# Kernel tuning notes

Measured on AMD Instinct MI355X. Metric: run time of the kernel, lower is better.

## Reference

```python
import math
import jax, jax.numpy as jnp
import numpy as np

EMBED_DIM = 2048
NUM_HEADS = 16
NUM_KV_HEADS = 8
DEPTH = 12
HEAD_DIM = EMBED_DIM // NUM_HEADS // 2  # 64
N_REP = NUM_HEADS // NUM_KV_HEADS       # 2
SCALING = HEAD_DIM ** (-0.5)
LAMBDA_INIT = 0.8 - 0.6 * math.exp(-0.3 * DEPTH)
EPS = 1e-5


def _rope_cos_sin(seq_len, head_dim, offset=0):
    pos = jnp.arange(offset, offset + seq_len, dtype=jnp.float32)
    theta = jnp.arange(0, head_dim, 2, dtype=jnp.float32) / head_dim
    inv_freq = 1.0 / (10000.0 ** theta + 1e-8)
    sinusoid = pos[:, None] * inv_freq[None, :]  # [seq, head_dim//2]
    return jnp.cos(sinusoid), jnp.sin(sinusoid)


def _apply_rotary_interleaved(x, cos, sin):
    # x: [b, s, h, d]; cos/sin: [s, d//2]; interleaved pairs (even, odd)
    x1 = x[..., 0::2]
    x2 = x[..., 1::2]
    c = cos[None, :, None, :]
    s = sin[None, :, None, :]
    o1 = x1 * c - x2 * s
    o2 = x1 * s + x2 * c
    return jnp.stack([o1, o2], axis=-1).reshape(x.shape)


def setup_inputs() -> dict:
    key = jax.random.key(0)
    ks = jax.random.split(key, 12)
    d = EMBED_DIM
    inp = {
        "q": jax.random.normal(ks[0], (1, 2048, d), dtype=jnp.float32),
        "k": jax.random.normal(ks[1], (1, 2048, d), dtype=jnp.float32),
        "v": jax.random.normal(ks[2], (1, 2048, d), dtype=jnp.float32),
        "Wq": jax.random.normal(ks[3], (d, d), dtype=jnp.float32) * (d ** -0.5),
        "Wk": jax.random.normal(ks[4], (d, d // N_REP), dtype=jnp.float32) * (d ** -0.5),
        "Wv": jax.random.normal(ks[5], (d, d // N_REP), dtype=jnp.float32) * (d ** -0.5),
        "Wout": jax.random.normal(ks[6], (d, d), dtype=jnp.float32) * (d ** -0.5),
        "lq1": jax.random.normal(ks[7], (HEAD_DIM,), dtype=jnp.float32) * 0.1,
        "lk1": jax.random.normal(ks[8], (HEAD_DIM,), dtype=jnp.float32) * 0.1,
        "lq2": jax.random.normal(ks[9], (HEAD_DIM,), dtype=jnp.float32) * 0.1,
        "lk2": jax.random.normal(ks[10], (HEAD_DIM,), dtype=jnp.float32) * 0.1,
        "subln_w": jnp.ones((2 * HEAD_DIM,), dtype=jnp.float32),
    }
    return inp


def reference(q, k, v, Wq, Wk, Wv, Wout, lq1, lk1, lq2, lk2, subln_w):
    bsz, tgt_len, _ = q.shape
    src_len = k.shape[1]
    hd = HEAD_DIM

    qp = (q @ Wq).reshape(bsz, tgt_len, 2 * NUM_HEADS, hd)
    kp = (k @ Wk).reshape(bsz, src_len, 2 * NUM_KV_HEADS, hd)
    vp = (v @ Wv).reshape(bsz, src_len, NUM_KV_HEADS, 2 * hd)

    q_cos, q_sin = _rope_cos_sin(tgt_len, hd)
    k_cos, k_sin = _rope_cos_sin(src_len, hd)
    qp = _apply_rotary_interleaved(qp, q_cos, q_sin)
    kp = _apply_rotary_interleaved(kp, k_cos, k_sin)

    qp = jnp.transpose(qp, (0, 2, 1, 3)) * SCALING          # [b, 2H, t, hd]
    kp = jnp.repeat(jnp.transpose(kp, (0, 2, 1, 3)), N_REP, axis=1)  # [b, 2H, s, hd]
    vp = jnp.repeat(jnp.transpose(vp, (0, 2, 1, 3)), N_REP, axis=1)  # [b, H, s, 2hd]

    attn_weights = jnp.einsum('bhtd,bhsd->bhts', qp, kp)
    attn_weights = jax.nn.softmax(attn_weights.astype(jnp.float32), axis=-1).astype(qp.dtype)

    lambda_1 = jnp.exp(jnp.sum(lq1 * lk1))
    lambda_2 = jnp.exp(jnp.sum(lq2 * lk2))
    lambda_full = lambda_1 - lambda_2 + LAMBDA_INIT

    attn_weights = attn_weights.reshape(bsz, NUM_HEADS, 2, tgt_len, src_len)
    attn_weights = attn_weights[:, :, 0] - lambda_full * attn_weights[:, :, 1]

    attn = jnp.einsum('bhts,bhsd->bhtd', attn_weights, vp)  # [b, H, t, 2hd]

    # RMSNorm over last dim with affine weight
    rms = jax.lax.rsqrt(jnp.mean(jnp.square(attn), axis=-1, keepdims=True) + EPS)
    attn = attn * rms * subln_w
    attn = attn * (1.0 - LAMBDA_INIT)

    attn = jnp.transpose(attn, (0, 2, 1, 3)).reshape(bsz, tgt_len, NUM_HEADS * 2 * hd)
    return attn @ Wout
```

## Files before the change

### kernel.cpp

```cpp
#include <hip/hip_runtime.h>

typedef unsigned short u16;
typedef unsigned int u32;
typedef float f32x4 __attribute__((ext_vector_type(4)));
typedef float f32x2 __attribute__((ext_vector_type(2)));
typedef unsigned int u32x2 __attribute__((ext_vector_type(2)));
typedef __bf16 bf16x8 __attribute__((ext_vector_type(8)));
typedef __bf16 bf16x4 __attribute__((ext_vector_type(4)));

#define LAMBDA_INIT_F 0.7836057665316245f
#define ONE_MINUS_LI  0.2163942334683755f
#define THR_LOG2 11.0f
#define Q_SCALE 0.18033688011112042f

__device__ __forceinline__ u16 f2b(float f) {
  union { float f; u32 u; } x; x.f = f;
  u32 r = x.u + 0x7fffu + ((x.u >> 16) & 1u);
  return (u16)(r >> 16);
}

__device__ __forceinline__ f32x4 mfma16(bf16x8 a, bf16x8 b, f32x4 c) {
  return __builtin_amdgcn_mfma_f32_16x16x32_bf16(a, b, c, 0, 0, 0);
}

__device__ __forceinline__ float fexp2(float x) { return __builtin_amdgcn_exp2f(x); }

__device__ __forceinline__ void gll16(const void* gp, void* lp) {
  __builtin_amdgcn_global_load_lds((__attribute__((address_space(1))) void*)(gp),
                                   (__attribute__((address_space(3))) void*)(lp),
                                   16, 0, 0);
}

__global__ __launch_bounds__(256) void cast3_kernel(const float* __restrict__ q,
                                                    const float* __restrict__ k,
                                                    const float* __restrict__ v,
                                                    u16* __restrict__ qb,
                                                    u16* __restrict__ kb,
                                                    u16* __restrict__ vb,
                                                    f32x2* __restrict__ tbl) {
  int bid = blockIdx.x;
  if (bid >= 6144) {
    int idx = (bid - 6144) * 256 + threadIdx.x;
    int t = idx >> 5, j = idx & 31;
    float theta = (float)j * (1.0f / 32.0f);
    float denom = expf(theta * 9.210340371976184f);
    float invf = 1.0f / (denom + 1e-8f);
    float ang = (float)t * invf;
    tbl[idx] = (f32x2){cosf(ang), sinf(ang)};
    return;
  }
  int seg = bid >> 11;
  int i = (bid & 2047) * 256 + threadIdx.x;
  const float* in = seg == 0 ? q : (seg == 1 ? k : v);
  u16* out = seg == 0 ? qb : (seg == 1 ? kb : vb);
  const f32x4* p = (const f32x4*)(in + (size_t)i * 8);
  f32x4 a = p[0], b = p[1];
  union { u16 u[8]; f32x4 v; } o;
#pragma unroll
  for (int j = 0; j < 4; ++j) { o.u[j] = f2b(a[j]); o.u[4 + j] = f2b(b[j]); }
  *(f32x4*)(out + (size_t)i * 8) = o.v;
}

__device__ __forceinline__ void trans_body(const float* __restrict__ in,
                                           u16* __restrict__ out, int R, int C) {
  __shared__ float tile[32][33];
  int bx = blockIdx.x * 32;
  int by = blockIdx.y * 32;
  int tx = threadIdx.x & 31, ty = threadIdx.x >> 5;
#pragma unroll
  for (int i = 0; i < 32; i += 8)
    tile[ty + i][tx] = in[(size_t)(by + ty + i) * C + bx + tx];
  __syncthreads();
#pragma unroll
  for (int i = 0; i < 32; i += 8)
    out[(size_t)(bx + ty + i) * R + by + tx] = f2b(tile[tx][ty + i]);
}

__global__ __launch_bounds__(256) void wtrans_kernel(
    const float* __restrict__ Wq, u16* __restrict__ WqT,
    const float* __restrict__ Wk, u16* __restrict__ WkT,
    const float* __restrict__ Wv, u16* __restrict__ WvT,
    const float* __restrict__ Wo, u16* __restrict__ WoT) {
  int z = blockIdx.z;
  const float* in;
  u16* out;
  int C;
  if (z == 0)      { in = Wq; out = WqT; C = 2048; }
  else if (z == 1) { in = Wk; out = WkT; C = 1024; }
  else if (z == 2) { in = Wv; out = WvT; C = 1024; }
  else             { in = Wo; out = WoT; C = 2048; }
  if (blockIdx.x * 32 >= C) return;
  trans_body(in, out, 2048, C);
}

template <int MODE>
__device__ __forceinline__ void gemm_body(u16* As, u16* Bs,
                                          const u16* __restrict__ A,
                                          const u16* __restrict__ Bt,
                                          void* __restrict__ Cout,
                                          const f32x2* __restrict__ tbl,
                                          float scale,
                                          int N, int K, int bx, int by) {
  const int tid = threadIdx.x;
  const int lane = tid & 63;
  const int wave = tid >> 6;
  const int m0 = by * 128;
  const int n0 = bx * 128;
  const int wm = (wave >> 1) * 64;
  const int wn = (wave & 1) * 64;
  const int g = lane >> 4, c = lane & 15;

  f32x4 acc[4][4];
#pragma unroll
  for (int i = 0; i < 4; ++i)
#pragma unroll
    for (int j = 0; j < 4; ++j) acc[i][j] = (f32x4){0.f, 0.f, 0.f, 0.f};

  for (int k0 = 0; k0 < K; k0 += 64) {
    __syncthreads();
#pragma unroll
    for (int it = 0; it < 4; ++it) {
      int gi = it * 256 + tid;
      int R = gi >> 3;
      int lg = (gi & 7) ^ (R & 7);
      gll16(A + (size_t)(m0 + R) * K + k0 + lg * 8, As + gi * 8);
      gll16(Bt + (size_t)(n0 + R) * K + k0 + lg * 8, Bs + gi * 8);
    }
    __syncthreads();
#pragma unroll
    for (int kk = 0; kk < 2; ++kk) {
      bf16x8 af[4], bf[4];
#pragma unroll
      for (int i = 0; i < 4; ++i) {
        int ph = ((kk * 4 + g) ^ (c & 7)) * 8;
        af[i] = *(const bf16x8*)&As[(wm + i * 16 + c) * 64 + ph];
        bf[i] = *(const bf16x8*)&Bs[(wn + i * 16 + c) * 64 + ph];
      }
#pragma unroll
      for (int i = 0; i < 4; ++i)
#pragma unroll
        for (int j = 0; j < 4; ++j) acc[i][j] = mfma16(af[i], bf[j], acc[i][j]);
    }
  }

  if constexpr (MODE == 0) {
    float* C = (float*)Cout;
#pragma unroll
    for (int i = 0; i < 4; ++i)
#pragma unroll
      for (int j = 0; j < 4; ++j) {
        int mrow = m0 + wm + i * 16 + g * 4;
        int ncol = n0 + wn + j * 16 + c;
#pragma unroll
        for (int r = 0; r < 4; ++r) C[(size_t)(mrow + r) * N + ncol] = acc[i][j][r];
      }
  } else if constexpr (MODE == 1) {
    u16* Oh = (u16*)Cout;
    const bool even = (c & 1) == 0;
#pragma unroll
    for (int i = 0; i < 4; ++i)
#pragma unroll
      for (int j = 0; j < 4; ++j) {
        int mrow = m0 + wm + i * 16 + g * 4;
        int ncol = n0 + wn + j * 16 + c;
        int hh = ncol >> 6;
        int d = ncol & 63;
        int jd = d >> 1;
        f32x4 own = acc[i][j];
        f32x4 part;
#pragma unroll
        for (int r = 0; r < 4; ++r) part[r] = __shfl_xor(own[r], 1);
        if (even) {
#pragma unroll
          for (int r = 0; r < 4; ++r) {
            f32x2 cs = tbl[(mrow + r) * 32 + jd];
            float o1 = (own[r] * cs[0] - part[r] * cs[1]) * scale;
            float o2 = (own[r] * cs[1] + part[r] * cs[0]) * scale;
            u32 pk = (u32)f2b(o1) | ((u32)f2b(o2) << 16);
            *(u32*)&Oh[((size_t)hh * 2048 + mrow + r) * 64 + d] = pk;
          }
        }
      }
  } else {
    u16* Vt = (u16*)Cout;
#pragma unroll
    for (int i = 0; i < 4; ++i)
#pragma unroll
      for (int j = 0; j < 4; ++j) {
        int ncol = n0 + wn + j * 16 + c;
        int tblk = (m0 + wm + i * 16) >> 5;
        int p0 = 8 * g + 4 * (i & 1);
        u32x2 pk;
        pk[0] = (u32)f2b(acc[i][j][0]) | ((u32)f2b(acc[i][j][1]) << 16);
        pk[1] = (u32)f2b(acc[i][j][2]) | ((u32)f2b(acc[i][j][3]) << 16);
        *(u32x2*)&Vt[(size_t)ncol * 2048 + tblk * 32 + p0] = pk;
      }
  }
}

__global__ __launch_bounds__(256, 2) void gemm_qkv_kernel(
    const u16* __restrict__ qb, const u16* __restrict__ WqT, u16* __restrict__ Qh,
    const u16* __restrict__ kb, const u16* __restrict__ WkT, u16* __restrict__ Kh,
    const u16* __restrict__ vb, const u16* __restrict__ WvT, u16* __restrict__ Vt,
    const f32x2* __restrict__ tbl) {
  __shared__ u16 As[128 * 64];
  __shared__ u16 Bs[128 * 64];
  int bid = ((blockIdx.x & 7) << 6) | (blockIdx.x >> 3);
  if (bid < 256) {
    gemm_body<1>(As, Bs, qb, WqT, Qh, tbl, Q_SCALE, 2048, 2048, bid & 15, bid >> 4);
  } else if (bid < 384) {
    int t = bid - 256;
    gemm_body<1>(As, Bs, kb, WkT, Kh, tbl, 1.0f, 1024, 2048, t & 7, t >> 3);
  } else {
    int t = bid - 384;
    gemm_body<2>(As, Bs, vb, WvT, Vt, tbl, 1.0f, 1024, 2048, t & 7, t >> 3);
  }
}

__global__ __launch_bounds__(256, 2) void gemm_one_kernel(const u16* __restrict__ A,
                                                          const u16* __restrict__ Bt,
                                                          float* __restrict__ C) {
  __shared__ u16 As[128 * 64];
  __shared__ u16 Bs[128 * 64];
  int bid = ((blockIdx.x & 7) << 5) | (blockIdx.x >> 3);
  gemm_body<0>(As, Bs, A, Bt, C, nullptr, 1.0f, 2048, 2048, bid & 15, bid >> 4);
}

__global__ __launch_bounds__(512, 2) void attn_kernel(const u16* __restrict__ Qb,
                                                      const u16* __restrict__ Kb,
                                                      const u16* __restrict__ Vt,
                                                      u16* __restrict__ AO,
                                                      const float* __restrict__ lq1,
                                                      const float* __restrict__ lk1,
                                                      const float* __restrict__ lq2,
                                                      const float* __restrict__ lk2,
                                                      const float* __restrict__ subln) {
  const int b = ((blockIdx.x & 7) << 5) | (blockIdx.x >> 3);
  const int h = b >> 4;
  const int tid = threadIdx.x;
  const int wave = tid >> 6;
  const int lane = tid & 63;
  const int t0 = ((b & 15) * 8 + wave) * 16;
  const int g = lane >> 4, c = lane & 15;
  const int c7 = c & 7;

  __shared__ u16 smem[24576];

  const u16* Kh = Kb + (size_t)h * 2048 * 64;
  const u16* Vh = Vt + (size_t)(h >> 1) * 128 * 2048;

  float myl1 = lq1[lane] * lk1[lane];
  float myl2 = lq2[lane] * lk2[lane];
#pragma unroll
  for (int off = 32; off; off >>= 1) {
    myl1 += __shfl_xor(myl1, off);
    myl2 += __shfl_xor(myl2, off);
  }
  const float lambda_full = expf(myl1) - expf(myl2) + LAMBDA_INIT_F;

  bf16x8 qf[2][2];
#pragma unroll
  for (int e = 0; e < 2; ++e)
#pragma unroll
    for (int d = 0; d < 2; ++d)
      qf[e][d] = *(const bf16x8*)(Qb + ((size_t)(2 * h + e) * 2048 + t0 + c) * 64 + d * 32 + g * 8);

  const int kb0 = c * 64 + ((g ^ c7) * 8);
  const int kb1 = kb0 ^ 32;

  const u16* ksrc0;
  const u16* vsrc0;
  const u16* vsrc1;
  { int gi = tid;       int R = gi >> 3; ksrc0 = Kh + R * 64 + ((gi & 7) ^ (R & 7)) * 8; }
  { int gi = tid;       int R = gi >> 3; vsrc0 = Vh + (size_t)R * 2048 + ((gi & 7) ^ (R & 7)) * 8; }
  { int gi = 512 + tid; int R = gi >> 3; vsrc1 = Vh + (size_t)R * 2048 + ((gi & 7) ^ (R & 7)) * 8; }

  f32x4 O[2][8];
#pragma unroll
  for (int e = 0; e < 2; ++e)
#pragma unroll
    for (int f = 0; f < 8; ++f) O[e][f] = (f32x4){0.f, 0.f, 0.f, 0.f};
  float m0 = -1e30f, m1 = -1e30f, ls0 = 0.f, ls1 = 0.f;

#define STAGE(kOff, vOff, s0)                                   \
  do {                                                          \
    gll16(ksrc0 + (size_t)(s0) * 64, smem + (kOff) + tid * 8);  \
    gll16(vsrc0 + (s0), smem + (vOff) + tid * 8);               \
    gll16(vsrc1 + (s0), smem + (vOff) + 4096 + tid * 8);        \
  } while (0)

#define TILE(kOff, vOff)                                                      \
  do {                                                                        \
    bf16x8 kf[4][2];                                                          \
    _Pragma("unroll") for (int sf = 0; sf < 4; ++sf) {                        \
      kf[sf][0] = *(const bf16x8*)&smem[(kOff) + kb0 + sf * 1024];            \
      kf[sf][1] = *(const bf16x8*)&smem[(kOff) + kb1 + sf * 1024];            \
    }                                                                         \
    f32x4 sa[2][4];                                                           \
    _Pragma("unroll") for (int e = 0; e < 2; ++e)                             \
      _Pragma("unroll") for (int sf = 0; sf < 4; ++sf) {                      \
        f32x4 z = (f32x4){0.f, 0.f, 0.f, 0.f};                                \
        z = mfma16(kf[sf][0], qf[e][0], z);                                   \
        z = mfma16(kf[sf][1], qf[e][1], z);                                   \
        sa[e][sf] = z;                                                        \
      }                                                                       \
    bf16x8 vv0[8];                                                            \
    _Pragma("unroll") for (int f = 0; f < 8; ++f)                             \
      vv0[f] = *(const bf16x8*)&smem[(vOff) + kb0 + f * 1024];                \
    bf16x8 paf[2][2];                                                         \
    _Pragma("unroll") for (int e = 0; e < 2; ++e) {                           \
      float& m_e = e ? m1 : m0;                                               \
      float& ls_e = e ? ls1 : ls0;                                            \
      float mx = sa[e][0][0];                                                 \
      _Pragma("unroll") for (int sf = 0; sf < 4; ++sf)                        \
        _Pragma("unroll") for (int r = 0; r < 4; ++r)                         \
          mx = fmaxf(mx, sa[e][sf][r]);                                       \
      mx = fmaxf(mx, __shfl_xor(mx, 16));                                     \
      mx = fmaxf(mx, __shfl_xor(mx, 32));                                     \
      if (__any(mx > m_e + THR_LOG2)) {                                       \
        float mn = fmaxf(m_e, mx);                                            \
        float sc = fexp2(m_e - mn);                                           \
        m_e = mn;                                                             \
        ls_e *= sc;                                                           \
        float scr[4];                                                         \
        _Pragma("unroll") for (int r = 0; r < 4; ++r) scr[r] = __shfl(sc, g * 4 + r); \
        _Pragma("unroll") for (int ff = 0; ff < 8; ++ff)                      \
          _Pragma("unroll") for (int r = 0; r < 4; ++r) O[e][ff][r] *= scr[r]; \
      }                                                                       \
      float p[4][4];                                                          \
      float sum = 0.f;                                                        \
      _Pragma("unroll") for (int sf = 0; sf < 4; ++sf)                        \
        _Pragma("unroll") for (int r = 0; r < 4; ++r) {                       \
          float pv = fexp2(sa[e][sf][r] - m_e);                               \
          p[sf][r] = pv;                                                      \
          sum += pv;                                                          \
        }                                                                     \
      sum += __shfl_xor(sum, 16);                                             \
      sum += __shfl_xor(sum, 32);                                             \
      ls_e += sum;                                                            \
      paf[e][0] = (bf16x8){(__bf16)p[0][0], (__bf16)p[0][1], (__bf16)p[0][2], (__bf16)p[0][3], \
                           (__bf16)p[1][0], (__bf16)p[1][1], (__bf16)p[1][2], (__bf16)p[1][3]}; \
      paf[e][1] = (bf16x8){(__bf16)p[2][0], (__bf16)p[2][1], (__bf16)p[2][2], (__bf16)p[2][3], \
                           (__bf16)p[3][0], (__bf16)p[3][1], (__bf16)p[3][2], (__bf16)p[3][3]}; \
    }                                                                         \
    __builtin_amdgcn_s_setprio(1);                                            \
    bf16x8 vv1[8];                                                            \
    _Pragma("unroll") for (int f = 0; f < 8; ++f)                             \
      vv1[f] = *(const bf16x8*)&smem[(vOff) + kb1 + f * 1024];                \
    _Pragma("unroll") for (int f = 0; f < 8; ++f) {                           \
      O[0][f] = mfma16(paf[0][0], vv0[f], O[0][f]);                           \
      O[1][f] = mfma16(paf[1][0], vv0[f], O[1][f]);                           \
    }                                                                         \
    _Pragma("unroll") for (int f = 0; f < 8; ++f) {                           \
      O[0][f] = mfma16(paf[0][1], vv1[f], O[0][f]);                           \
      O[1][f] = mfma16(paf[1][1], vv1[f], O[1][f]);                           \
    }                                                                         \
    __builtin_amdgcn_s_setprio(0);                                            \
  } while (0)

  STAGE(0, 8192, 0);

#pragma unroll 1
  for (int t = 0; t < 32; t += 2) {
    __syncthreads();
    STAGE(4096, 16384, (t + 1) * 64);
    TILE(0, 8192);
    __syncthreads();
    if (t < 30) STAGE(0, 8192, (t + 2) * 64);
    TILE(4096, 16384);
  }

  float inv0 = 1.f / ls0, inv1 = 1.f / ls1;
  float i0[4], i1[4];
#pragma unroll
  for (int r = 0; r < 4; ++r) {
    i0[r] = __shfl(inv0, g * 4 + r);
    i1[r] = __shfl(inv1, g * 4 + r);
  }
  float res[8][4];
  float ss[4] = {0.f, 0.f, 0.f, 0.f};
#pragma unroll
  for (int f = 0; f < 8; ++f)
#pragma unroll
    for (int r = 0; r < 4; ++r) {
      float vv = O[0][f][r] * i0[r] - lambda_full * (O[1][f][r] * i1[r]);
      res[f][r] = vv;
      ss[r] += vv * vv;
    }
#pragma unroll
  for (int off = 1; off < 16; off <<= 1)
#pragma unroll
    for (int r = 0; r < 4; ++r) ss[r] += __shfl_xor(ss[r], off);
  float rms[4];
#pragma unroll
  for (int r = 0; r < 4; ++r)
    rms[r] = rsqrtf(ss[r] * (1.0f / 128.0f) + 1e-5f) * ONE_MINUS_LI;
  float w[8];
#pragma unroll
  for (int f = 0; f < 8; ++f) w[f] = subln[f * 16 + c];
#pragma unroll
  for (int f = 0; f < 8; ++f)
#pragma unroll
    for (int r = 0; r < 4; ++r)
      AO[(size_t)(t0 + g * 4 + r) * 2048 + h * 128 + f * 16 + c] = f2b(res[f][r] * rms[r] * w[f]);
}

extern "C" void kernel_launch(void* const* d_in, const int* in_sizes, int n_in,
                              void* d_out, int out_size, void* d_ws, size_t ws_size,
                              hipStream_t stream) {
  const float* q     = (const float*)d_in[0];
  const float* k     = (const float*)d_in[1];
  const float* v     = (const float*)d_in[2];
  const float* Wq    = (const float*)d_in[3];
  const float* Wk    = (const float*)d_in[4];
  const float* Wv    = (const float*)d_in[5];
  const float* Wout  = (const float*)d_in[6];
  const float* lq1   = (const float*)d_in[7];
  const float* lk1   = (const float*)d_in[8];
  const float* lq2   = (const float*)d_in[9];
  const float* lk2   = (const float*)d_in[10];
  const float* subln = (const float*)d_in[11];
  float* out = (float*)d_out;

  char* ws = (char*)d_ws;
  size_t off = 0;
  auto alloc = [&](size_t bytes) -> void* {
    void* p = ws + off;
    off += (bytes + 255) & ~(size_t)255;
    return p;
  };
  u16* qb  = (u16*)alloc(2048ull * 2048 * 2);
  u16* kb  = (u16*)alloc(2048ull * 2048 * 2);
  u16* vb  = (u16*)alloc(2048ull * 2048 * 2);
  u16* WqT = (u16*)alloc(2048ull * 2048 * 2);
  u16* WkT = (u16*)alloc(1024ull * 2048 * 2);
  u16* WvT = (u16*)alloc(1024ull * 2048 * 2);
  u16* WoT = (u16*)alloc(2048ull * 2048 * 2);
  f32x2* tbl = (f32x2*)alloc(2048ull * 32 * 8);
  u16* Qh  = (u16*)alloc(32ull * 2048 * 64 * 2);
  u16* Kh  = (u16*)alloc(16ull * 2048 * 64 * 2);
  u16* Vt  = (u16*)alloc(1024ull * 2048 * 2);
  u16* AO  = (u16*)alloc(2048ull * 2048 * 2);

  cast3_kernel<<<6400, 256, 0, stream>>>(q, k, v, qb, kb, vb, tbl);
  wtrans_kernel<<<dim3(64, 64, 4), 256, 0, stream>>>(Wq, WqT, Wk, WkT, Wv, WvT, Wout, WoT);
  gemm_qkv_kernel<<<512, 256, 0, stream>>>(qb, WqT, Qh, kb, WkT, Kh, vb, WvT, Vt, tbl);
  attn_kernel<<<256, 512, 0, stream>>>(Qh, Kh, Vt, AO, lq1, lk1, lq2, lk2, subln);
  gemm_one_kernel<<<256, 256, 0, stream>>>(AO, WoT, out);
}
```

Before: 156.2 us.

## Merge prep kernels and split attention into smaller 4-wave blocks

The input cast, RoPE table and weight-transpose kernels are merged into a single prep launch, removing one kernel launch and the idle wasted blocks of the old 3D transpose grid. The attention kernel now runs 512 blocks of 256 threads, each covering 64 query rows instead of 128, with staging loads spread over four waves. This gives finer scheduling granularity across CUs, but each block now loads K/V tiles for half as many queries, doubling total K/V traffic.

```diff
diff --git a/kernel.cpp b/kernel.cpp
--- a/kernel.cpp
+++ b/kernel.cpp
@@ -31,15 +31,45 @@
                                    16, 0, 0);
 }
 
-__global__ __launch_bounds__(256) void cast3_kernel(const float* __restrict__ q,
-                                                    const float* __restrict__ k,
-                                                    const float* __restrict__ v,
-                                                    u16* __restrict__ qb,
-                                                    u16* __restrict__ kb,
-                                                    u16* __restrict__ vb,
-                                                    f32x2* __restrict__ tbl) {
+__device__ __forceinline__ void trans_body2(const float* __restrict__ in,
+                                            u16* __restrict__ out, int R, int C,
+                                            int bxb, int byb) {
+  __shared__ float tile[32][33];
+  int bx = bxb * 32;
+  int by = byb * 32;
+  int tx = threadIdx.x & 31, ty = threadIdx.x >> 5;
+#pragma unroll
+  for (int i = 0; i < 32; i += 8)
+    tile[ty + i][tx] = in[(size_t)(by + ty + i) * C + bx + tx];
+  __syncthreads();
+#pragma unroll
+  for (int i = 0; i < 32; i += 8)
+    out[(size_t)(bx + ty + i) * R + by + tx] = f2b(tile[tx][ty + i]);
+}
+
+__global__ __launch_bounds__(256) void prep_kernel(
+    const float* __restrict__ q, const float* __restrict__ k, const float* __restrict__ v,
+    u16* __restrict__ qb, u16* __restrict__ kb, u16* __restrict__ vb,
+    f32x2* __restrict__ tbl,
+    const float* __restrict__ Wq, u16* __restrict__ WqT,
+    const float* __restrict__ Wk, u16* __restrict__ WkT,
+    const float* __restrict__ Wv, u16* __restrict__ WvT,
+    const float* __restrict__ Wo, u16* __restrict__ WoT) {
   int bid = blockIdx.x;
-  if (bid >= 6144) {
+  if (bid < 6144) {
+    int seg = bid >> 11;
+    int i = (bid & 2047) * 256 + threadIdx.x;
+    const float* in = seg == 0 ? q : (seg == 1 ? k : v);
+    u16* out = seg == 0 ? qb : (seg == 1 ? kb : vb);
+    const f32x4* p = (const f32x4*)(in + (size_t)i * 8);
+    f32x4 a = p[0], b = p[1];
+    union { u16 u[8]; f32x4 v; } o;
+#pragma unroll
+    for (int j = 0; j < 4; ++j) { o.u[j] = f2b(a[j]); o.u[4 + j] = f2b(b[j]); }
+    *(f32x4*)(out + (size_t)i * 8) = o.v;
+    return;
+  }
+  if (bid < 6400) {
     int idx = (bid - 6144) * 256 + threadIdx.x;
     int t = idx >> 5, j = idx & 31;
     float theta = (float)j * (1.0f / 32.0f);
@@ -49,48 +79,11 @@
     tbl[idx] = (f32x2){cosf(ang), sinf(ang)};
     return;
   }
-  int seg = bid >> 11;
-  int i = (bid & 2047) * 256 + threadIdx.x;
-  const float* in = seg == 0 ? q : (seg == 1 ? k : v);
-  u16* out = seg == 0 ? qb : (seg == 1 ? kb : vb);
-  const f32x4* p = (const f32x4*)(in + (size_t)i * 8);
-  f32x4 a = p[0], b = p[1];
-  union { u16 u[8]; f32x4 v; } o;
-#pragma unroll
-  for (int j = 0; j < 4; ++j) { o.u[j] = f2b(a[j]); o.u[4 + j] = f2b(b[j]); }
-  *(f32x4*)(out + (size_t)i * 8) = o.v;
-}
-
-__device__ __forceinline__ void trans_body(const float* __restrict__ in,
-                                           u16* __restrict__ out, int R, int C) {
-  __shared__ float tile[32][33];
-  int bx = blockIdx.x * 32;
-  int by = blockIdx.y * 32;
-  int tx = threadIdx.x & 31, ty = threadIdx.x >> 5;
-#pragma unroll
-  for (int i = 0; i < 32; i += 8)
-    tile[ty + i][tx] = in[(size_t)(by + ty + i) * C + bx + tx];
-  __syncthreads();
-#pragma unroll
-  for (int i = 0; i < 32; i += 8)
-    out[(size_t)(bx + ty + i) * R + by + tx] = f2b(tile[tx][ty + i]);
-}
-
-__global__ __launch_bounds__(256) void wtrans_kernel(
-    const float* __restrict__ Wq, u16* __restrict__ WqT,
-    const float* __restrict__ Wk, u16* __restrict__ WkT,
-    const float* __restrict__ Wv, u16* __restrict__ WvT,
-    const float* __restrict__ Wo, u16* __restrict__ WoT) {
-  int z = blockIdx.z;
-  const float* in;
-  u16* out;
-  int C;
-  if (z == 0)      { in = Wq; out = WqT; C = 2048; }
-  else if (z == 1) { in = Wk; out = WkT; C = 1024; }
-  else if (z == 2) { in = Wv; out = WvT; C = 1024; }
-  else             { in = Wo; out = WoT; C = 2048; }
-  if (blockIdx.x * 32 >= C) return;
-  trans_body(in, out, 2048, C);
+  int w = bid - 6400;
+  if (w < 4096)      trans_body2(Wq, WqT, 2048, 2048, w & 63, w >> 6);
+  else if (w < 6144) { w -= 4096; trans_body2(Wk, WkT, 2048, 1024, w & 31, w >> 5); }
+  else if (w < 8192) { w -= 6144; trans_body2(Wv, WvT, 2048, 1024, w & 31, w >> 5); }
+  else               { w -= 8192; trans_body2(Wo, WoT, 2048, 2048, w & 63, w >> 6); }
 }
 
 template <int MODE>
@@ -226,7 +219,7 @@
   gemm_body<0>(As, Bs, A, Bt, C, nullptr, 1.0f, 2048, 2048, bid & 15, bid >> 4);
 }
 
-__global__ __launch_bounds__(512, 2) void attn_kernel(const u16* __restrict__ Qb,
+__global__ __launch_bounds__(256, 2) void attn_kernel(const u16* __restrict__ Qb,
                                                       const u16* __restrict__ Kb,
                                                       const u16* __restrict__ Vt,
                                                       u16* __restrict__ AO,
@@ -235,12 +228,12 @@
                                                       const float* __restrict__ lq2,
                                                       const float* __restrict__ lk2,
                                                       const float* __restrict__ subln) {
-  const int b = ((blockIdx.x & 7) << 5) | (blockIdx.x >> 3);
-  const int h = b >> 4;
+  const int b = ((blockIdx.x & 7) << 6) | (blockIdx.x >> 3);
+  const int h = b >> 5;
   const int tid = threadIdx.x;
   const int wave = tid >> 6;
   const int lane = tid & 63;
-  const int t0 = ((b & 15) * 8 + wave) * 16;
+  const int t0 = ((b & 31) * 4 + wave) * 16;
   const int g = lane >> 4, c = lane & 15;
   const int c7 = c & 7;
 
@@ -269,11 +262,17 @@
   const int kb1 = kb0 ^ 32;
 
   const u16* ksrc0;
+  const u16* ksrc1;
   const u16* vsrc0;
   const u16* vsrc1;
+  const u16* vsrc2;
+  const u16* vsrc3;
   { int gi = tid;       int R = gi >> 3; ksrc0 = Kh + R * 64 + ((gi & 7) ^ (R & 7)) * 8; }
+  { int gi = 256 + tid; int R = gi >> 3; ksrc1 = Kh + R * 64 + ((gi & 7) ^ (R & 7)) * 8; }
   { int gi = tid;       int R = gi >> 3; vsrc0 = Vh + (size_t)R * 2048 + ((gi & 7) ^ (R & 7)) * 8; }
-  { int gi = 512 + tid; int R = gi >> 3; vsrc1 = Vh + (size_t)R * 2048 + ((gi & 7) ^ (R & 7)) * 8; }
+  { int gi = 256 + tid; int R = gi >> 3; vsrc1 = Vh + (size_t)R * 2048 + ((gi & 7) ^ (R & 7)) * 8; }
+  { int gi = 512 + tid; int R = gi >> 3; vsrc2 = Vh + (size_t)R * 2048 + ((gi & 7) ^ (R & 7)) * 8; }
+  { int gi = 768 + tid; int R = gi >> 3; vsrc3 = Vh + (size_t)R * 2048 + ((gi & 7) ^ (R & 7)) * 8; }
 
   f32x4 O[2][8];
 #pragma unroll
@@ -282,11 +281,14 @@
     for (int f = 0; f < 8; ++f) O[e][f] = (f32x4){0.f, 0.f, 0.f, 0.f};
   float m0 = -1e30f, m1 = -1e30f, ls0 = 0.f, ls1 = 0.f;
 
-#define STAGE(kOff, vOff, s0)                                   \
-  do {                                                          \
-    gll16(ksrc0 + (size_t)(s0) * 64, smem + (kOff) + tid * 8);  \
-    gll16(vsrc0 + (s0), smem + (vOff) + tid * 8);               \
-    gll16(vsrc1 + (s0), smem + (vOff) + 4096 + tid * 8);        \
+#define STAGE(kOff, vOff, s0)                                         \
+  do {                                                                \
+    gll16(ksrc0 + (size_t)(s0) * 64, smem + (kOff) + tid * 8);        \
+    gll16(ksrc1 + (size_t)(s0) * 64, smem + (kOff) + 2048 + tid * 8); \
+    gll16(vsrc0 + (s0), smem + (vOff) + tid * 8);                     \
+    gll16(vsrc1 + (s0), smem + (vOff) + 2048 + tid * 8);              \
+    gll16(vsrc2 + (s0), smem + (vOff) + 4096 + tid * 8);              \
+    gll16(vsrc3 + (s0), smem + (vOff) + 6144 + tid * 8);              \
   } while (0)
 
 #define TILE(kOff, vOff)                                                      \
@@ -442,9 +444,9 @@
   u16* Vt  = (u16*)alloc(1024ull * 2048 * 2);
   u16* AO  = (u16*)alloc(2048ull * 2048 * 2);
 
-  cast3_kernel<<<6400, 256, 0, stream>>>(q, k, v, qb, kb, vb, tbl);
-  wtrans_kernel<<<dim3(64, 64, 4), 256, 0, stream>>>(Wq, WqT, Wk, WkT, Wv, WvT, Wout, WoT);
+  prep_kernel<<<18688, 256, 0, stream>>>(q, k, v, qb, kb, vb, tbl,
+                                         Wq, WqT, Wk, WkT, Wv, WvT, Wout, WoT);
   gemm_qkv_kernel<<<512, 256, 0, stream>>>(qb, WqT, Qh, kb, WkT, Kh, vb, WvT, Vt, tbl);
-  attn_kernel<<<256, 512, 0, stream>>>(Qh, Kh, Vt, AO, lq1, lk1, lq2, lk2, subln);
+  attn_kernel<<<512, 256, 0, stream>>>(Qh, Kh, Vt, AO, lq1, lk1, lq2, lk2, subln);
   gemm_one_kernel<<<256, 256, 0, stream>>>(AO, WoT, out);
 }
```

Result: no change. 159.0 us (+1.8%).
